# Kernel optimization log

Measured on AMD Instinct MI355X. Metric: run time of the kernel, lower is better.

## Reference

```python
import jax, jax.numpy as jnp
import numpy as np

DIM = 768
NUM_HEADS = 12
HEAD_DIM = DIM // NUM_HEADS
BASE = 10000.0


def rotate_half(x):
    x1, x2 = jnp.split(x, 2, axis=-1)
    return jnp.concatenate((-x2, x1), axis=-1)


def rope_cos_sin(seq_len, dim, dtype):
    inv_freq = 1.0 / (BASE ** (jnp.arange(0, dim, 2, dtype=jnp.float32) / dim))
    t = jnp.arange(seq_len, dtype=jnp.float32)
    freqs = jnp.einsum('i,j->ij', t, inv_freq)  # [N, dim/2]
    emb = jnp.concatenate((freqs, freqs), axis=-1)  # [N, dim]
    return jnp.cos(emb).astype(dtype), jnp.sin(emb).astype(dtype)


def setup_inputs() -> dict:
    key = jax.random.key(0)
    k1, k2, k3, k4 = jax.random.split(key, 4)
    B, N, C = 1, 4096, DIM
    x = jax.random.normal(k1, (B, N, C), dtype=jnp.float32)
    s = 1.0 / np.sqrt(C)
    qkv_w = jax.random.normal(k2, (3 * C, C), dtype=jnp.float32) * s
    proj_w = jax.random.normal(k3, (C, C), dtype=jnp.float32) * s
    proj_b = jax.random.normal(k4, (C,), dtype=jnp.float32) * 0.01
    return {"x": x, "qkv_w": qkv_w, "proj_w": proj_w, "proj_b": proj_b}


def reference(x, qkv_w, proj_w, proj_b):
    B, N, C = x.shape
    H, D = NUM_HEADS, HEAD_DIM
    scale = D ** -0.5
    qkv = jnp.einsum('bnc,oc->bno', x, qkv_w)           # [B, N, 3C]
    qkv = qkv.reshape(B, N, 3, H, D).transpose(2, 0, 3, 1, 4)  # [3, B, H, N, D]
    q, k, v = qkv[0], qkv[1], qkv[2]
    cos, sin = rope_cos_sin(N, D, x.dtype)              # [N, D] each
    cos = cos[None, None]                               # [1,1,N,D]
    sin = sin[None, None]
    q = q * cos + rotate_half(q) * sin
    k = k * cos + rotate_half(k) * sin
    attn = jnp.einsum('bhqd,bhkd->bhqk', q, k) * scale  # [B,H,N,N]
    attn = jax.nn.softmax(attn, axis=-1)
    out = jnp.einsum('bhqk,bhkd->bhqd', attn, v)        # [B,H,N,D]
    out = out.transpose(0, 2, 1, 3).reshape(B, N, C)
    return jnp.einsum('bnc,oc->bno', out, proj_w) + proj_b
```

## Files before the change

kernel.cpp:

```cpp
#include <hip/hip_runtime.h>
#include <hip/hip_bf16.h>
#include <math.h>

#define DIM 768
#define NHEADS 12
#define HD 64
#define SEQ 4096
#define KSPLIT 2

typedef __bf16 bf16x8 __attribute__((ext_vector_type(8)));
typedef float f32x4 __attribute__((ext_vector_type(4)));
typedef uint  u32x4 __attribute__((ext_vector_type(4)));

__device__ inline ushort f2bf(float f) {
    __bf16 b = (__bf16)f;
    union { __bf16 b; ushort u; } v; v.b = b;
    return v.u;
}

__device__ inline uint cvt_pk_bf16(float lo, float hi) {
    uint r;
    asm("v_cvt_pk_bf16_f32 %0, %1, %2" : "=v"(r) : "v"(lo), "v"(hi));
    return r;
}

__device__ inline void gload16(const ushort* gsrc, ushort* lbase) {
    __builtin_amdgcn_global_load_lds(
        (const __attribute__((address_space(1))) uint*)gsrc,
        (__attribute__((address_space(3))) uint*)lbase, 16, 0, 0);
}

__global__ __launch_bounds__(256)
void prep(const float* __restrict__ x, const float* __restrict__ qkv_w,
          const float* __restrict__ proj_w,
          ushort* __restrict__ xb, ushort* __restrict__ qwb,
          ushort* __restrict__ pwb, float2* __restrict__ tab)
{
    const int b = blockIdx.x;
    if (b < 5376) {
        const float* src; ushort* dst; int i;
        if (b < 3072)      { src = x;      dst = xb;  i = b * 256 + threadIdx.x; }
        else if (b < 4800) { src = qkv_w;  dst = qwb; i = (b - 3072) * 256 + threadIdx.x; }
        else               { src = proj_w; dst = pwb; i = (b - 4800) * 256 + threadIdx.x; }
        const float4 v = ((const float4*)src)[i];
        ushort4 w;
        w.x = f2bf(v.x); w.y = f2bf(v.y); w.z = f2bf(v.z); w.w = f2bf(v.w);
        ((ushort4*)dst)[i] = w;
    } else {
        const int idx = (b - 5376) * 256 + threadIdx.x;
        const int j = idx & 31;
        const int n = idx >> 5;
        const float invf = (float)pow(10000.0, -(double)j / 32.0);
        const float ang  = (float)n * invf;
        double s, c;
        sincos((double)ang, &s, &c);
        tab[idx] = make_float2((float)c, (float)s);
    }
}

__global__ __launch_bounds__(256)
void gemm_qkv(const ushort* __restrict__ A, const ushort* __restrict__ B,
              const float2* __restrict__ tab,
              ushort* __restrict__ Qb, ushort* __restrict__ Kb,
              ushort* __restrict__ Vp)
{
    constexpr int BM = 128, BN = 128, BK = 64;
    __shared__ __attribute__((aligned(16))) ushort Ah[2][BM][BK];
    __shared__ __attribute__((aligned(16))) ushort Bh[2][BN][BK];

    const int t    = threadIdx.x;
    const int lane = t & 63;
    const int wv   = t >> 6;
    const int wm   = (wv >> 1) * 64;
    const int wn   = (wv & 1) * 64;
    const int m0   = blockIdx.y * BM;
    const int n0   = blockIdx.x * BN;

    f32x4 acc[4][4] = {};

    const int lrow = lane >> 3;
    const int lch  = (lane & 7) * 8;

    #pragma unroll
    for (int i = 0; i < 4; ++i) {
        const int rb = i * 32 + wv * 8;
        gload16(&A[(size_t)(m0 + rb + lrow) * DIM + lch], &Ah[0][rb][0]);
        gload16(&B[(size_t)(n0 + rb + lrow) * DIM + lch], &Bh[0][rb][0]);
    }
    __syncthreads();

    int cur = 0;
    for (int k0 = 0; k0 < DIM; k0 += BK) {
        if (k0 + BK < DIM) {
            #pragma unroll
            for (int i = 0; i < 4; ++i) {
                const int rb = i * 32 + wv * 8;
                gload16(&A[(size_t)(m0 + rb + lrow) * DIM + k0 + BK + lch],
                        &Ah[cur ^ 1][rb][0]);
                gload16(&B[(size_t)(n0 + rb + lrow) * DIM + k0 + BK + lch],
                        &Bh[cur ^ 1][rb][0]);
            }
        }

        #pragma unroll
        for (int ks = 0; ks < BK; ks += 32) {
            const int koff = ks + ((lane >> 4) << 3);
            const int rs = lane & 15;
            bf16x8 af[4], bf[4];
            #pragma unroll
            for (int i = 0; i < 4; ++i) {
                af[i] = *(const bf16x8*)&Ah[cur][wm + i * 16 + rs][koff];
                bf[i] = *(const bf16x8*)&Bh[cur][wn + i * 16 + rs][koff];
            }
            #pragma unroll
            for (int i = 0; i < 4; ++i)
                #pragma unroll
                for (int j = 0; j < 4; ++j)
                    acc[i][j] = __builtin_amdgcn_mfma_f32_16x16x32_bf16(
                        af[i], bf[j], acc[i][j], 0, 0, 0);
        }
        __syncthreads();
        cur ^= 1;
    }

    const int rsel  = lane & 15;
    const int quad  = lane >> 4;
    const int rbase = m0 + wm + (quad << 2);
    const int c0    = n0 + wn;
    const int tt    = c0 / DIM;
    const int h     = (c0 % DIM) >> 6;

    if (tt == 2) {
        const int T = (m0 + wm) >> 6;
        #pragma unroll
        for (int j = 0; j < 4; ++j) {
            const int d = rsel + 16 * j;
            ushort vvA[8], vvB[8];
            #pragma unroll
            for (int i2 = 0; i2 < 2; ++i2)
                #pragma unroll
                for (int r = 0; r < 4; ++r) {
                    vvA[4 * i2 + r] = f2bf(acc[i2][j][r]);
                    vvB[4 * i2 + r] = f2bf(acc[2 + i2][j][r]);
                }
            ushort* dst = &Vp[((size_t)h * HD + d) * SEQ + T * 64];
            *(float4*)&dst[8 * quad]      = *(const float4*)&vvA[0];
            *(float4*)&dst[32 + 8 * quad] = *(const float4*)&vvB[0];
        }
    } else {
        ushort* dstb = (tt == 0 ? Qb : Kb) + (size_t)h * SEQ * HD;
        const float qs = (tt == 0) ? 0.18033688011112042f : 1.0f;
        #pragma unroll
        for (int i = 0; i < 4; ++i)
            #pragma unroll
            for (int r = 0; r < 4; ++r) {
                const int n = rbase + i * 16 + r;
                #pragma unroll
                for (int j = 0; j < 2; ++j) {
                    const float a = acc[i][j][r];
                    const float b = acc[i][j + 2][r];
                    const float2 cs2 = tab[n * 32 + rsel + 16 * j];
                    dstb[(size_t)n * HD + rsel + 16 * j]      = f2bf((a * cs2.x - b * cs2.y) * qs);
                    dstb[(size_t)n * HD + rsel + 16 * j + 32] = f2bf((b * cs2.x + a * cs2.y) * qs);
                }
            }
    }
}

__global__ __launch_bounds__(256, 2)
void flash_mfma(const ushort* __restrict__ Qb, const ushort* __restrict__ Kb,
                const ushort* __restrict__ Vp,
                float* __restrict__ Opart, float* __restrict__ lpart)
{
    __shared__ ushort Ks[2][64][68];
    __shared__ ushort Vs[2][64][68];

    const int t    = threadIdx.x;
    const int lane = t & 63;
    const int wv   = t >> 6;
    const int rsel = lane & 15;
    const int quad = lane >> 4;

    const int p  = blockIdx.x + 32 * (blockIdx.y + 12 * blockIdx.z);
    const int c  = p & 7;
    const int r  = p >> 3;
    const int gi = r >> 5;
    const int xq = r & 31;
    const int g  = gi * 8 + c;
    const int h    = g % 12;
    const int part = g / 12;

    const int q0   = xq * 128 + wv * 32;
    const int Tbeg = (part * (SEQ / KSPLIT)) >> 6;
    const int Tend = Tbeg + (SEQ / KSPLIT) / 64;

    const int crow = t >> 2;
    const int ccol = (t & 3) * 16;

    bf16x8 aq[2][2];
    #pragma unroll
    for (int mi = 0; mi < 2; ++mi)
        #pragma unroll
        for (int ks = 0; ks < 2; ++ks)
            aq[mi][ks] = *(const bf16x8*)&Qb[((size_t)h * SEQ + q0 + 16 * mi + rsel) * HD
                                             + ks * 32 + quad * 8];

    const u32x4 onesw = { 0x3F803F80u, 0x3F803F80u, 0x3F803F80u, 0x3F803F80u };
    const bf16x8 ones = __builtin_bit_cast(bf16x8, onesw);

    f32x4 accO[2][4] = {};
    f32x4 accL[2] = {};

    {
        const ushort* ksrc = &Kb[((size_t)h * SEQ + Tbeg * 64 + crow) * HD + ccol];
        const float4 k0 = *(const float4*)&ksrc[0];
        const float4 k1 = *(const float4*)&ksrc[8];
        const ushort* vsrc = &Vp[((size_t)h * HD + crow) * SEQ + Tbeg * 64 + ccol];
        const float4 v0 = *(const float4*)&vsrc[0];
        const float4 v1 = *(const float4*)&vsrc[8];
        *(float4*)&Ks[0][crow][ccol]     = k0;
        *(float4*)&Ks[0][crow][ccol + 8] = k1;
        *(float4*)&Vs[0][crow][ccol]     = v0;
        *(float4*)&Vs[0][crow][ccol + 8] = v1;
    }
    __syncthreads();

    int cur = 0;
    for (int T = Tbeg; T < Tend; ++T) {
        const int Tn = (T + 1 < Tend) ? T + 1 : T;
        const ushort* ksrc = &Kb[((size_t)h * SEQ + Tn * 64 + crow) * HD + ccol];
        const float4 kn0 = *(const float4*)&ksrc[0];
        const float4 kn1 = *(const float4*)&ksrc[8];
        const ushort* vsrc = &Vp[((size_t)h * HD + crow) * SEQ + Tn * 64 + ccol];
        const float4 vn0 = *(const float4*)&vsrc[0];
        const float4 vn1 = *(const float4*)&vsrc[8];

        f32x4 accS[2][4] = {};
        __builtin_amdgcn_s_setprio(1);
        #pragma unroll
        for (int ks = 0; ks < 2; ++ks)
            #pragma unroll
            for (int n = 0; n < 4; ++n) {
                const bf16x8 bk =
                    *(const bf16x8*)&Ks[cur][16 * n + rsel][32 * ks + quad * 8];
                accS[0][n] = __builtin_amdgcn_mfma_f32_16x16x32_bf16(
                    bk, aq[0][ks], accS[0][n], 0, 0, 0);
                accS[1][n] = __builtin_amdgcn_mfma_f32_16x16x32_bf16(
                    bk, aq[1][ks], accS[1][n], 0, 0, 0);
            }
        __builtin_amdgcn_s_setprio(0);

        bf16x8 ap[2][2];
        #pragma unroll
        for (int mi = 0; mi < 2; ++mi) {
            const float p00 = __builtin_amdgcn_exp2f(accS[mi][0][0]);
            const float p01 = __builtin_amdgcn_exp2f(accS[mi][0][1]);
            const float p02 = __builtin_amdgcn_exp2f(accS[mi][0][2]);
            const float p03 = __builtin_amdgcn_exp2f(accS[mi][0][3]);
            const float p10 = __builtin_amdgcn_exp2f(accS[mi][1][0]);
            const float p11 = __builtin_amdgcn_exp2f(accS[mi][1][1]);
            const float p12 = __builtin_amdgcn_exp2f(accS[mi][1][2]);
            const float p13 = __builtin_amdgcn_exp2f(accS[mi][1][3]);
            const float p20 = __builtin_amdgcn_exp2f(accS[mi][2][0]);
            const float p21 = __builtin_amdgcn_exp2f(accS[mi][2][1]);
            const float p22 = __builtin_amdgcn_exp2f(accS[mi][2][2]);
            const float p23 = __builtin_amdgcn_exp2f(accS[mi][2][3]);
            const float p30 = __builtin_amdgcn_exp2f(accS[mi][3][0]);
            const float p31 = __builtin_amdgcn_exp2f(accS[mi][3][1]);
            const float p32 = __builtin_amdgcn_exp2f(accS[mi][3][2]);
            const float p33 = __builtin_amdgcn_exp2f(accS[mi][3][3]);

            const u32x4 aw0 = { cvt_pk_bf16(p00, p01), cvt_pk_bf16(p02, p03),
                                cvt_pk_bf16(p10, p11), cvt_pk_bf16(p12, p13) };
            const u32x4 aw1 = { cvt_pk_bf16(p20, p21), cvt_pk_bf16(p22, p23),
                                cvt_pk_bf16(p30, p31), cvt_pk_bf16(p32, p33) };
            ap[mi][0] = __builtin_bit_cast(bf16x8, aw0);
            ap[mi][1] = __builtin_bit_cast(bf16x8, aw1);
        }

        __builtin_amdgcn_s_setprio(1);
        #pragma unroll
        for (int j = 0; j < 4; ++j) {
            const bf16x8 bv0 = *(const bf16x8*)&Vs[cur][16 * j + rsel][quad * 8];
            const bf16x8 bv1 = *(const bf16x8*)&Vs[cur][16 * j + rsel][32 + quad * 8];
            accO[0][j] = __builtin_amdgcn_mfma_f32_16x16x32_bf16(
                ap[0][0], bv0, accO[0][j], 0, 0, 0);
            accO[0][j] = __builtin_amdgcn_mfma_f32_16x16x32_bf16(
                ap[0][1], bv1, accO[0][j], 0, 0, 0);
            accO[1][j] = __builtin_amdgcn_mfma_f32_16x16x32_bf16(
                ap[1][0], bv0, accO[1][j], 0, 0, 0);
            accO[1][j] = __builtin_amdgcn_mfma_f32_16x16x32_bf16(
                ap[1][1], bv1, accO[1][j], 0, 0, 0);
        }
        #pragma unroll
        for (int mi = 0; mi < 2; ++mi) {
            accL[mi] = __builtin_amdgcn_mfma_f32_16x16x32_bf16(
                ap[mi][0], ones, accL[mi], 0, 0, 0);
            accL[mi] = __builtin_amdgcn_mfma_f32_16x16x32_bf16(
                ap[mi][1], ones, accL[mi], 0, 0, 0);
        }
        __builtin_amdgcn_s_setprio(0);

        *(float4*)&Ks[cur ^ 1][crow][ccol]     = kn0;
        *(float4*)&Ks[cur ^ 1][crow][ccol + 8] = kn1;
        *(float4*)&Vs[cur ^ 1][crow][ccol]     = vn0;
        *(float4*)&Vs[cur ^ 1][crow][ccol + 8] = vn1;
        __syncthreads();
        cur ^= 1;
    }

    float* Ob = Opart + ((size_t)part * NHEADS + h) * SEQ * HD;
    float* lb = lpart + ((size_t)part * NHEADS + h) * SEQ;
    #pragma unroll
    for (int mi = 0; mi < 2; ++mi)
        #pragma unroll
        for (int r = 0; r < 4; ++r) {
            const int n = q0 + 16 * mi + 4 * quad + r;
            #pragma unroll
            for (int j = 0; j < 4; ++j)
                Ob[(size_t)n * HD + 16 * j + rsel] = accO[mi][j][r];
            if (rsel == 0) lb[n] = accL[mi][r];
        }
}

__global__ __launch_bounds__(256)
void merge_k(const float* __restrict__ Opart, const float* __restrict__ lpart,
             ushort* __restrict__ AO)
{
    const int idx = blockIdx.x * 256 + threadIdx.x;
    const int dg = idx & 15;
    const int n  = (idx >> 4) & (SEQ - 1);
    const int h  = idx >> 16;

    float4 o = make_float4(0.f, 0.f, 0.f, 0.f);
    float l = 0.f;
    #pragma unroll
    for (int p = 0; p < KSPLIT; ++p) {
        const float4 v = *(const float4*)&Opart[(((size_t)p * NHEADS + h) * SEQ + n) * HD + dg * 4];
        o.x += v.x; o.y += v.y; o.z += v.z; o.w += v.w;
        l += lpart[((size_t)p * NHEADS + h) * SEQ + n];
    }
    const float inv = 1.f / l;
    ushort4 w;
    w.x = f2bf(o.x * inv); w.y = f2bf(o.y * inv);
    w.z = f2bf(o.z * inv); w.w = f2bf(o.w * inv);
    *(ushort4*)&AO[(size_t)n * DIM + h * HD + dg * 4] = w;
}

__global__ __launch_bounds__(256)
void gemm_proj(const ushort* __restrict__ A, const ushort* __restrict__ B,
               const float* __restrict__ bias, float* __restrict__ out)
{
    constexpr int BM = 128, BN = 128, BK = 64;
    __shared__ __attribute__((aligned(16))) ushort As[2][BM][BK];
    __shared__ __attribute__((aligned(16))) ushort Bs[2][BN][BK];

    const int t    = threadIdx.x;
    const int lane = t & 63;
    const int wv   = t >> 6;
    const int wm   = (wv >> 1) * 64;
    const int wn   = (wv & 1) * 64;
    const int m0   = blockIdx.y * BM;
    const int n0   = blockIdx.x * BN;

    f32x4 acc[4][4] = {};

    const int lrow = lane >> 3;
    const int lch  = (lane & 7) * 8;

    #pragma unroll
    for (int i = 0; i < 4; ++i) {
        const int rb = i * 32 + wv * 8;
        gload16(&A[(size_t)(m0 + rb + lrow) * DIM + lch], &As[0][rb][0]);
        gload16(&B[(size_t)(n0 + rb + lrow) * DIM + lch], &Bs[0][rb][0]);
    }
    __syncthreads();

    int cur = 0;
    for (int k0 = 0; k0 < DIM; k0 += BK) {
        if (k0 + BK < DIM) {
            #pragma unroll
            for (int i = 0; i < 4; ++i) {
                const int rb = i * 32 + wv * 8;
                gload16(&A[(size_t)(m0 + rb + lrow) * DIM + k0 + BK + lch],
                        &As[cur ^ 1][rb][0]);
                gload16(&B[(size_t)(n0 + rb + lrow) * DIM + k0 + BK + lch],
                        &Bs[cur ^ 1][rb][0]);
            }
        }

        #pragma unroll
        for (int ks = 0; ks < BK; ks += 32) {
            const int koff = ks + ((lane >> 4) << 3);
            const int rs = lane & 15;
            bf16x8 af[4], bf[4];
            #pragma unroll
            for (int i = 0; i < 4; ++i) {
                af[i] = *(const bf16x8*)&As[cur][wm + i * 16 + rs][koff];
                bf[i] = *(const bf16x8*)&Bs[cur][wn + i * 16 + rs][koff];
            }
            #pragma unroll
            for (int i = 0; i < 4; ++i)
                #pragma unroll
                for (int j = 0; j < 4; ++j)
                    acc[i][j] = __builtin_amdgcn_mfma_f32_16x16x32_bf16(
                        af[i], bf[j], acc[i][j], 0, 0, 0);
        }
        __syncthreads();
        cur ^= 1;
    }

    const int rbase = m0 + wm + ((lane >> 4) << 2);
    const int cbase = n0 + wn + (lane & 15);

    #pragma unroll
    for (int j = 0; j < 4; ++j) {
        const int col = cbase + j * 16;
        const float bv = bias[col];
        #pragma unroll
        for (int i = 0; i < 4; ++i) {
            const int row0 = rbase + i * 16;
            #pragma unroll
            for (int r = 0; r < 4; ++r)
                out[(size_t)(row0 + r) * DIM + col] = acc[i][j][r] + bv;
        }
    }
}

extern "C" void kernel_launch(void* const* d_in, const int* in_sizes, int n_in,
                              void* d_out, int out_size, void* d_ws, size_t ws_size,
                              hipStream_t stream)
{
    const float* x      = (const float*)d_in[0];
    const float* qkv_w  = (const float*)d_in[1];
    const float* proj_w = (const float*)d_in[2];
    const float* proj_b = (const float*)d_in[3];

    const size_t headsz = (size_t)NHEADS * SEQ * HD;
    char* p = (char*)d_ws;
    ushort* Qb    = (ushort*)p;                 p += headsz * 2;
    ushort* Kb    = (ushort*)p;                 p += headsz * 2;
    ushort* Vp    = (ushort*)p;                 p += headsz * 2;
    ushort* AO    = (ushort*)p;                 p += (size_t)SEQ * DIM * 2;
    float*  Opart = (float*)p;                  p += (size_t)KSPLIT * headsz * 4;
    float*  lpart = (float*)p;                  p += (size_t)KSPLIT * NHEADS * SEQ * 4;
    float2* tab   = (float2*)p;                 p += (size_t)SEQ * 32 * sizeof(float2);
    ushort* xb    = (ushort*)p;                 p += (size_t)SEQ * DIM * 2;
    ushort* qwb   = (ushort*)p;                 p += (size_t)3 * DIM * DIM * 2;
    ushort* pwb   = (ushort*)p;
    float*  out   = (float*)d_out;

    prep<<<5888, 256, 0, stream>>>(x, qkv_w, proj_w, xb, qwb, pwb, tab);

    gemm_qkv<<<dim3(3 * DIM / 128, SEQ / 128), 256, 0, stream>>>(
        xb, qwb, tab, Qb, Kb, Vp);

    flash_mfma<<<dim3(SEQ / 128, NHEADS, KSPLIT), 256, 0, stream>>>(
        Qb, Kb, Vp, Opart, lpart);

    merge_k<<<(NHEADS * SEQ * 16) / 256, 256, 0, stream>>>(Opart, lpart, AO);

    gemm_proj<<<dim3(DIM / 128, SEQ / 128), 256, 0, stream>>>(
        AO, pwb, proj_b, out);
}
```

Before: 190.1 us.

## Fuse split-K merge into projection GEMM A-loading and tidy flash prefetch

Removes the separate merge kernel: the projection GEMM now reads both split-K partial outputs and row sums, normalises and converts to bf16 while staging the A tile into shared memory. The block index is remapped so groups of blocks share row tiles, which should improve L2 reuse. In the flash kernel, K fragments are preloaded into registers before the MFMA loop, and the redundant final prefetch and barrier are skipped. This saves one launch and the AO write/read round trip, but A staging now goes through registers with fp32 loads at twice the bytes instead of async direct loads, which may stall the GEMM pipeline.

```diff
diff --git a/kernel.cpp b/kernel.cpp
--- a/kernel.cpp
+++ b/kernel.cpp
@@ -227,13 +227,23 @@
 
     int cur = 0;
     for (int T = Tbeg; T < Tend; ++T) {
-        const int Tn = (T + 1 < Tend) ? T + 1 : T;
-        const ushort* ksrc = &Kb[((size_t)h * SEQ + Tn * 64 + crow) * HD + ccol];
-        const float4 kn0 = *(const float4*)&ksrc[0];
-        const float4 kn1 = *(const float4*)&ksrc[8];
-        const ushort* vsrc = &Vp[((size_t)h * HD + crow) * SEQ + Tn * 64 + ccol];
-        const float4 vn0 = *(const float4*)&vsrc[0];
-        const float4 vn1 = *(const float4*)&vsrc[8];
+        const bool more = (T + 1 < Tend);
+        float4 kn0, kn1, vn0, vn1;
+        if (more) {
+            const ushort* ksrc = &Kb[((size_t)h * SEQ + (T + 1) * 64 + crow) * HD + ccol];
+            kn0 = *(const float4*)&ksrc[0];
+            kn1 = *(const float4*)&ksrc[8];
+            const ushort* vsrc = &Vp[((size_t)h * HD + crow) * SEQ + (T + 1) * 64 + ccol];
+            vn0 = *(const float4*)&vsrc[0];
+            vn1 = *(const float4*)&vsrc[8];
+        }
+
+        bf16x8 bk[4][2];
+        #pragma unroll
+        for (int n = 0; n < 4; ++n)
+            #pragma unroll
+            for (int ks = 0; ks < 2; ++ks)
+                bk[n][ks] = *(const bf16x8*)&Ks[cur][16 * n + rsel][32 * ks + quad * 8];
 
         f32x4 accS[2][4] = {};
         __builtin_amdgcn_s_setprio(1);
@@ -241,12 +251,10 @@
         for (int ks = 0; ks < 2; ++ks)
             #pragma unroll
             for (int n = 0; n < 4; ++n) {
-                const bf16x8 bk =
-                    *(const bf16x8*)&Ks[cur][16 * n + rsel][32 * ks + quad * 8];
                 accS[0][n] = __builtin_amdgcn_mfma_f32_16x16x32_bf16(
-                    bk, aq[0][ks], accS[0][n], 0, 0, 0);
+                    bk[n][ks], aq[0][ks], accS[0][n], 0, 0, 0);
                 accS[1][n] = __builtin_amdgcn_mfma_f32_16x16x32_bf16(
-                    bk, aq[1][ks], accS[1][n], 0, 0, 0);
+                    bk[n][ks], aq[1][ks], accS[1][n], 0, 0, 0);
             }
         __builtin_amdgcn_s_setprio(0);
 
@@ -301,12 +309,14 @@
         }
         __builtin_amdgcn_s_setprio(0);
 
-        *(float4*)&Ks[cur ^ 1][crow][ccol]     = kn0;
-        *(float4*)&Ks[cur ^ 1][crow][ccol + 8] = kn1;
-        *(float4*)&Vs[cur ^ 1][crow][ccol]     = vn0;
-        *(float4*)&Vs[cur ^ 1][crow][ccol + 8] = vn1;
-        __syncthreads();
-        cur ^= 1;
+        if (more) {
+            *(float4*)&Ks[cur ^ 1][crow][ccol]     = kn0;
+            *(float4*)&Ks[cur ^ 1][crow][ccol + 8] = kn1;
+            *(float4*)&Vs[cur ^ 1][crow][ccol]     = vn0;
+            *(float4*)&Vs[cur ^ 1][crow][ccol + 8] = vn1;
+            __syncthreads();
+            cur ^= 1;
+        }
     }
 
     float* Ob = Opart + ((size_t)part * NHEADS + h) * SEQ * HD;
@@ -324,34 +334,12 @@
 }
 
 __global__ __launch_bounds__(256)
-void merge_k(const float* __restrict__ Opart, const float* __restrict__ lpart,
-             ushort* __restrict__ AO)
-{
-    const int idx = blockIdx.x * 256 + threadIdx.x;
-    const int dg = idx & 15;
-    const int n  = (idx >> 4) & (SEQ - 1);
-    const int h  = idx >> 16;
-
-    float4 o = make_float4(0.f, 0.f, 0.f, 0.f);
-    float l = 0.f;
-    #pragma unroll
-    for (int p = 0; p < KSPLIT; ++p) {
-        const float4 v = *(const float4*)&Opart[(((size_t)p * NHEADS + h) * SEQ + n) * HD + dg * 4];
-        o.x += v.x; o.y += v.y; o.z += v.z; o.w += v.w;
-        l += lpart[((size_t)p * NHEADS + h) * SEQ + n];
-    }
-    const float inv = 1.f / l;
-    ushort4 w;
-    w.x = f2bf(o.x * inv); w.y = f2bf(o.y * inv);
-    w.z = f2bf(o.z * inv); w.w = f2bf(o.w * inv);
-    *(ushort4*)&AO[(size_t)n * DIM + h * HD + dg * 4] = w;
-}
-
-__global__ __launch_bounds__(256)
-void gemm_proj(const ushort* __restrict__ A, const ushort* __restrict__ B,
-               const float* __restrict__ bias, float* __restrict__ out)
+void gemm_proj(const float* __restrict__ Opart, const float* __restrict__ lpart,
+               const ushort* __restrict__ B, const float* __restrict__ bias,
+               float* __restrict__ out)
 {
     constexpr int BM = 128, BN = 128, BK = 64;
+    constexpr size_t HSZ = (size_t)NHEADS * SEQ * HD;
     __shared__ __attribute__((aligned(16))) ushort As[2][BM][BK];
     __shared__ __attribute__((aligned(16))) ushort Bs[2][BN][BK];
 
@@ -360,18 +348,45 @@
     const int wv   = t >> 6;
     const int wm   = (wv >> 1) * 64;
     const int wn   = (wv & 1) * 64;
-    const int m0   = blockIdx.y * BM;
-    const int n0   = blockIdx.x * BN;
+
+    const int p   = blockIdx.x + 6 * blockIdx.y;
+    const int c   = p & 7;
+    const int r   = p >> 3;
+    const int xb_ = r % 6;
+    const int yb_ = c * 4 + r / 6;
+    const int m0  = yb_ * BM;
+    const int n0  = xb_ * BN;
 
     f32x4 acc[4][4] = {};
 
     const int lrow = lane >> 3;
     const int lch  = (lane & 7) * 8;
 
+    auto stageA = [&](int buf, int k0) {
+        const int hh = k0 >> 6;
+        #pragma unroll
+        for (int i = 0; i < 4; ++i) {
+            const int n_ = m0 + i * 32 + wv * 8 + lrow;
+            const size_t base = ((size_t)hh * SEQ + n_) * HD + lch;
+            const float4 a0 = *(const float4*)&Opart[base];
+            const float4 a1 = *(const float4*)&Opart[base + 4];
+            const float4 b0 = *(const float4*)&Opart[HSZ + base];
+            const float4 b1 = *(const float4*)&Opart[HSZ + base + 4];
+            const float inv = 1.f / (lpart[(size_t)hh * SEQ + n_]
+                                   + lpart[(size_t)NHEADS * SEQ + (size_t)hh * SEQ + n_]);
+            const u32x4 aw = {
+                (uint)f2bf((a0.x + b0.x) * inv) | ((uint)f2bf((a0.y + b0.y) * inv) << 16),
+                (uint)f2bf((a0.z + b0.z) * inv) | ((uint)f2bf((a0.w + b0.w) * inv) << 16),
+                (uint)f2bf((a1.x + b1.x) * inv) | ((uint)f2bf((a1.y + b1.y) * inv) << 16),
+                (uint)f2bf((a1.z + b1.z) * inv) | ((uint)f2bf((a1.w + b1.w) * inv) << 16) };
+            *(u32x4*)&As[buf][i * 32 + wv * 8 + lrow][lch] = aw;
+        }
+    };
+
+    stageA(0, 0);
     #pragma unroll
     for (int i = 0; i < 4; ++i) {
         const int rb = i * 32 + wv * 8;
-        gload16(&A[(size_t)(m0 + rb + lrow) * DIM + lch], &As[0][rb][0]);
         gload16(&B[(size_t)(n0 + rb + lrow) * DIM + lch], &Bs[0][rb][0]);
     }
     __syncthreads();
@@ -379,11 +394,10 @@
     int cur = 0;
     for (int k0 = 0; k0 < DIM; k0 += BK) {
         if (k0 + BK < DIM) {
+            stageA(cur ^ 1, k0 + BK);
             #pragma unroll
             for (int i = 0; i < 4; ++i) {
                 const int rb = i * 32 + wv * 8;
-                gload16(&A[(size_t)(m0 + rb + lrow) * DIM + k0 + BK + lch],
-                        &As[cur ^ 1][rb][0]);
                 gload16(&B[(size_t)(n0 + rb + lrow) * DIM + k0 + BK + lch],
                         &Bs[cur ^ 1][rb][0]);
             }
@@ -421,8 +435,8 @@
         for (int i = 0; i < 4; ++i) {
             const int row0 = rbase + i * 16;
             #pragma unroll
-            for (int r = 0; r < 4; ++r)
-                out[(size_t)(row0 + r) * DIM + col] = acc[i][j][r] + bv;
+            for (int r2 = 0; r2 < 4; ++r2)
+                out[(size_t)(row0 + r2) * DIM + col] = acc[i][j][r2] + bv;
         }
     }
 }
@@ -449,6 +463,7 @@
     ushort* qwb   = (ushort*)p;                 p += (size_t)3 * DIM * DIM * 2;
     ushort* pwb   = (ushort*)p;
     float*  out   = (float*)d_out;
+    (void)AO;
 
     prep<<<5888, 256, 0, stream>>>(x, qkv_w, proj_w, xb, qwb, pwb, tab);
 
@@ -458,8 +473,6 @@
     flash_mfma<<<dim3(SEQ / 128, NHEADS, KSPLIT), 256, 0, stream>>>(
         Qb, Kb, Vp, Opart, lpart);
 
-    merge_k<<<(NHEADS * SEQ * 16) / 256, 256, 0, stream>>>(Opart, lpart, AO);
-
     gemm_proj<<<dim3(DIM / 128, SEQ / 128), 256, 0, stream>>>(
-        AO, pwb, proj_b, out);
-}
+        Opart, lpart, pwb, proj_b, out);
+}
```

Result: slower. 200.5 us (+5.5%).

## Process two KV tiles per barrier with a four-slot LDS ring

Applied to the files above, without the earlier changes.

The flash attention loop now handles two 64-key tiles per iteration using a 4-slot shared-memory ring (two pairs), prefetching the next two tiles into registers before computing. This halves the number of __syncthreads barriers and gives global loads twice as much compute to hide behind. The cost is double the LDS footprint (about 70KB per block) and more live prefetch registers, which may limit the two-blocks-per-CU occupancy target.

```diff
diff --git a/kernel.cpp b/kernel.cpp
--- a/kernel.cpp
+++ b/kernel.cpp
@@ -172,8 +172,8 @@
                 const ushort* __restrict__ Vp,
                 float* __restrict__ Opart, float* __restrict__ lpart)
 {
-    __shared__ ushort Ks[2][64][68];
-    __shared__ ushort Vs[2][64][68];
+    __shared__ ushort Ks[4][64][68];
+    __shared__ ushort Vs[4][64][68];
 
     const int t    = threadIdx.x;
     const int lane = t & 63;
@@ -211,102 +211,119 @@
     f32x4 accO[2][4] = {};
     f32x4 accL[2] = {};
 
-    {
-        const ushort* ksrc = &Kb[((size_t)h * SEQ + Tbeg * 64 + crow) * HD + ccol];
+    #pragma unroll
+    for (int s = 0; s < 2; ++s) {
+        const ushort* ksrc = &Kb[((size_t)h * SEQ + (Tbeg + s) * 64 + crow) * HD + ccol];
         const float4 k0 = *(const float4*)&ksrc[0];
         const float4 k1 = *(const float4*)&ksrc[8];
-        const ushort* vsrc = &Vp[((size_t)h * HD + crow) * SEQ + Tbeg * 64 + ccol];
+        const ushort* vsrc = &Vp[((size_t)h * HD + crow) * SEQ + (Tbeg + s) * 64 + ccol];
         const float4 v0 = *(const float4*)&vsrc[0];
         const float4 v1 = *(const float4*)&vsrc[8];
-        *(float4*)&Ks[0][crow][ccol]     = k0;
-        *(float4*)&Ks[0][crow][ccol + 8] = k1;
-        *(float4*)&Vs[0][crow][ccol]     = v0;
-        *(float4*)&Vs[0][crow][ccol + 8] = v1;
+        *(float4*)&Ks[s][crow][ccol]     = k0;
+        *(float4*)&Ks[s][crow][ccol + 8] = k1;
+        *(float4*)&Vs[s][crow][ccol]     = v0;
+        *(float4*)&Vs[s][crow][ccol + 8] = v1;
     }
     __syncthreads();
 
     int cur = 0;
-    for (int T = Tbeg; T < Tend; ++T) {
-        const int Tn = (T + 1 < Tend) ? T + 1 : T;
-        const ushort* ksrc = &Kb[((size_t)h * SEQ + Tn * 64 + crow) * HD + ccol];
-        const float4 kn0 = *(const float4*)&ksrc[0];
-        const float4 kn1 = *(const float4*)&ksrc[8];
-        const ushort* vsrc = &Vp[((size_t)h * HD + crow) * SEQ + Tn * 64 + ccol];
-        const float4 vn0 = *(const float4*)&vsrc[0];
-        const float4 vn1 = *(const float4*)&vsrc[8];
-
-        f32x4 accS[2][4] = {};
-        __builtin_amdgcn_s_setprio(1);
-        #pragma unroll
-        for (int ks = 0; ks < 2; ++ks)
-            #pragma unroll
-            for (int n = 0; n < 4; ++n) {
-                const bf16x8 bk =
-                    *(const bf16x8*)&Ks[cur][16 * n + rsel][32 * ks + quad * 8];
-                accS[0][n] = __builtin_amdgcn_mfma_f32_16x16x32_bf16(
-                    bk, aq[0][ks], accS[0][n], 0, 0, 0);
-                accS[1][n] = __builtin_amdgcn_mfma_f32_16x16x32_bf16(
-                    bk, aq[1][ks], accS[1][n], 0, 0, 0);
-            }
-        __builtin_amdgcn_s_setprio(0);
-
-        bf16x8 ap[2][2];
-        #pragma unroll
-        for (int mi = 0; mi < 2; ++mi) {
-            const float p00 = __builtin_amdgcn_exp2f(accS[mi][0][0]);
-            const float p01 = __builtin_amdgcn_exp2f(accS[mi][0][1]);
-            const float p02 = __builtin_amdgcn_exp2f(accS[mi][0][2]);
-            const float p03 = __builtin_amdgcn_exp2f(accS[mi][0][3]);
-            const float p10 = __builtin_amdgcn_exp2f(accS[mi][1][0]);
-            const float p11 = __builtin_amdgcn_exp2f(accS[mi][1][1]);
-            const float p12 = __builtin_amdgcn_exp2f(accS[mi][1][2]);
-            const float p13 = __builtin_amdgcn_exp2f(accS[mi][1][3]);
-            const float p20 = __builtin_amdgcn_exp2f(accS[mi][2][0]);
-            const float p21 = __builtin_amdgcn_exp2f(accS[mi][2][1]);
-            const float p22 = __builtin_amdgcn_exp2f(accS[mi][2][2]);
-            const float p23 = __builtin_amdgcn_exp2f(accS[mi][2][3]);
-            const float p30 = __builtin_amdgcn_exp2f(accS[mi][3][0]);
-            const float p31 = __builtin_amdgcn_exp2f(accS[mi][3][1]);
-            const float p32 = __builtin_amdgcn_exp2f(accS[mi][3][2]);
-            const float p33 = __builtin_amdgcn_exp2f(accS[mi][3][3]);
-
-            const u32x4 aw0 = { cvt_pk_bf16(p00, p01), cvt_pk_bf16(p02, p03),
-                                cvt_pk_bf16(p10, p11), cvt_pk_bf16(p12, p13) };
-            const u32x4 aw1 = { cvt_pk_bf16(p20, p21), cvt_pk_bf16(p22, p23),
-                                cvt_pk_bf16(p30, p31), cvt_pk_bf16(p32, p33) };
-            ap[mi][0] = __builtin_bit_cast(bf16x8, aw0);
-            ap[mi][1] = __builtin_bit_cast(bf16x8, aw1);
-        }
-
-        __builtin_amdgcn_s_setprio(1);
-        #pragma unroll
-        for (int j = 0; j < 4; ++j) {
-            const bf16x8 bv0 = *(const bf16x8*)&Vs[cur][16 * j + rsel][quad * 8];
-            const bf16x8 bv1 = *(const bf16x8*)&Vs[cur][16 * j + rsel][32 + quad * 8];
-            accO[0][j] = __builtin_amdgcn_mfma_f32_16x16x32_bf16(
-                ap[0][0], bv0, accO[0][j], 0, 0, 0);
-            accO[0][j] = __builtin_amdgcn_mfma_f32_16x16x32_bf16(
-                ap[0][1], bv1, accO[0][j], 0, 0, 0);
-            accO[1][j] = __builtin_amdgcn_mfma_f32_16x16x32_bf16(
-                ap[1][0], bv0, accO[1][j], 0, 0, 0);
-            accO[1][j] = __builtin_amdgcn_mfma_f32_16x16x32_bf16(
-                ap[1][1], bv1, accO[1][j], 0, 0, 0);
-        }
-        #pragma unroll
-        for (int mi = 0; mi < 2; ++mi) {
-            accL[mi] = __builtin_amdgcn_mfma_f32_16x16x32_bf16(
-                ap[mi][0], ones, accL[mi], 0, 0, 0);
-            accL[mi] = __builtin_amdgcn_mfma_f32_16x16x32_bf16(
-                ap[mi][1], ones, accL[mi], 0, 0, 0);
-        }
-        __builtin_amdgcn_s_setprio(0);
-
-        *(float4*)&Ks[cur ^ 1][crow][ccol]     = kn0;
-        *(float4*)&Ks[cur ^ 1][crow][ccol + 8] = kn1;
-        *(float4*)&Vs[cur ^ 1][crow][ccol]     = vn0;
-        *(float4*)&Vs[cur ^ 1][crow][ccol + 8] = vn1;
+    for (int T = Tbeg; T < Tend; T += 2) {
+        const int Tn0 = (T + 2 < Tend) ? T + 2 : T;
+        const int Tn1 = (T + 3 < Tend) ? T + 3 : T;
+        const ushort* kApt = &Kb[((size_t)h * SEQ + Tn0 * 64 + crow) * HD + ccol];
+        const float4 kA0 = *(const float4*)&kApt[0];
+        const float4 kA1 = *(const float4*)&kApt[8];
+        const ushort* vApt = &Vp[((size_t)h * HD + crow) * SEQ + Tn0 * 64 + ccol];
+        const float4 vA0 = *(const float4*)&vApt[0];
+        const float4 vA1 = *(const float4*)&vApt[8];
+        const ushort* kBpt = &Kb[((size_t)h * SEQ + Tn1 * 64 + crow) * HD + ccol];
+        const float4 kB0 = *(const float4*)&kBpt[0];
+        const float4 kB1 = *(const float4*)&kBpt[8];
+        const ushort* vBpt = &Vp[((size_t)h * HD + crow) * SEQ + Tn1 * 64 + ccol];
+        const float4 vB0 = *(const float4*)&vBpt[0];
+        const float4 vB1 = *(const float4*)&vBpt[8];
+
+        #pragma unroll
+        for (int sub = 0; sub < 2; ++sub) {
+            const int b = cur + sub;
+
+            f32x4 accS[2][4] = {};
+            __builtin_amdgcn_s_setprio(1);
+            #pragma unroll
+            for (int ks = 0; ks < 2; ++ks)
+                #pragma unroll
+                for (int n = 0; n < 4; ++n) {
+                    const bf16x8 bk =
+                        *(const bf16x8*)&Ks[b][16 * n + rsel][32 * ks + quad * 8];
+                    accS[0][n] = __builtin_amdgcn_mfma_f32_16x16x32_bf16(
+                        bk, aq[0][ks], accS[0][n], 0, 0, 0);
+                    accS[1][n] = __builtin_amdgcn_mfma_f32_16x16x32_bf16(
+                        bk, aq[1][ks], accS[1][n], 0, 0, 0);
+                }
+            __builtin_amdgcn_s_setprio(0);
+
+            bf16x8 ap[2][2];
+            #pragma unroll
+            for (int mi = 0; mi < 2; ++mi) {
+                const float p00 = __builtin_amdgcn_exp2f(accS[mi][0][0]);
+                const float p01 = __builtin_amdgcn_exp2f(accS[mi][0][1]);
+                const float p02 = __builtin_amdgcn_exp2f(accS[mi][0][2]);
+                const float p03 = __builtin_amdgcn_exp2f(accS[mi][0][3]);
+                const float p10 = __builtin_amdgcn_exp2f(accS[mi][1][0]);
+                const float p11 = __builtin_amdgcn_exp2f(accS[mi][1][1]);
+                const float p12 = __builtin_amdgcn_exp2f(accS[mi][1][2]);
+                const float p13 = __builtin_amdgcn_exp2f(accS[mi][1][3]);
+                const float p20 = __builtin_amdgcn_exp2f(accS[mi][2][0]);
+                const float p21 = __builtin_amdgcn_exp2f(accS[mi][2][1]);
+                const float p22 = __builtin_amdgcn_exp2f(accS[mi][2][2]);
+                const float p23 = __builtin_amdgcn_exp2f(accS[mi][2][3]);
+                const float p30 = __builtin_amdgcn_exp2f(accS[mi][3][0]);
+                const float p31 = __builtin_amdgcn_exp2f(accS[mi][3][1]);
+                const float p32 = __builtin_amdgcn_exp2f(accS[mi][3][2]);
+                const float p33 = __builtin_amdgcn_exp2f(accS[mi][3][3]);
+
+                const u32x4 aw0 = { cvt_pk_bf16(p00, p01), cvt_pk_bf16(p02, p03),
+                                    cvt_pk_bf16(p10, p11), cvt_pk_bf16(p12, p13) };
+                const u32x4 aw1 = { cvt_pk_bf16(p20, p21), cvt_pk_bf16(p22, p23),
+                                    cvt_pk_bf16(p30, p31), cvt_pk_bf16(p32, p33) };
+                ap[mi][0] = __builtin_bit_cast(bf16x8, aw0);
+                ap[mi][1] = __builtin_bit_cast(bf16x8, aw1);
+            }
+
+            __builtin_amdgcn_s_setprio(1);
+            #pragma unroll
+            for (int j = 0; j < 4; ++j) {
+                const bf16x8 bv0 = *(const bf16x8*)&Vs[b][16 * j + rsel][quad * 8];
+                const bf16x8 bv1 = *(const bf16x8*)&Vs[b][16 * j + rsel][32 + quad * 8];
+                accO[0][j] = __builtin_amdgcn_mfma_f32_16x16x32_bf16(
+                    ap[0][0], bv0, accO[0][j], 0, 0, 0);
+                accO[0][j] = __builtin_amdgcn_mfma_f32_16x16x32_bf16(
+                    ap[0][1], bv1, accO[0][j], 0, 0, 0);
+                accO[1][j] = __builtin_amdgcn_mfma_f32_16x16x32_bf16(
+                    ap[1][0], bv0, accO[1][j], 0, 0, 0);
+                accO[1][j] = __builtin_amdgcn_mfma_f32_16x16x32_bf16(
+                    ap[1][1], bv1, accO[1][j], 0, 0, 0);
+            }
+            #pragma unroll
+            for (int mi = 0; mi < 2; ++mi) {
+                accL[mi] = __builtin_amdgcn_mfma_f32_16x16x32_bf16(
+                    ap[mi][0], ones, accL[mi], 0, 0, 0);
+                accL[mi] = __builtin_amdgcn_mfma_f32_16x16x32_bf16(
+                    ap[mi][1], ones, accL[mi], 0, 0, 0);
+            }
+            __builtin_amdgcn_s_setprio(0);
+        }
+
+        *(float4*)&Ks[cur ^ 2][crow][ccol]           = kA0;
+        *(float4*)&Ks[cur ^ 2][crow][ccol + 8]       = kA1;
+        *(float4*)&Vs[cur ^ 2][crow][ccol]           = vA0;
+        *(float4*)&Vs[cur ^ 2][crow][ccol + 8]       = vA1;
+        *(float4*)&Ks[(cur ^ 2) + 1][crow][ccol]     = kB0;
+        *(float4*)&Ks[(cur ^ 2) + 1][crow][ccol + 8] = kB1;
+        *(float4*)&Vs[(cur ^ 2) + 1][crow][ccol]     = vB0;
+        *(float4*)&Vs[(cur ^ 2) + 1][crow][ccol + 8] = vB1;
         __syncthreads();
-        cur ^= 1;
+        cur ^= 2;
     }
 
     float* Ob = Opart + ((size_t)part * NHEADS + h) * SEQ * HD;
```

Result: slower. 195.8 us (+3.0%).
